# Kernel optimization log

Hardware: AMD Instinct MI355X
Metric: run time of the kernel (lower is better)

Reference implementation:

```python
import jax, jax.numpy as jnp
import numpy as np
from jax import lax

HID = 1024   # hidden_size
NH = 16      # num_heads
NKV = 4      # num_kv_heads (GQA)
HD = 64      # head_dim
SPLIT = 64   # fixed attention split size
KS = 3       # dynamic conv kernel size


def setup_inputs() -> dict:
    key = jax.random.key(0)
    ks = jax.random.split(key, 9)
    s = 0.02
    return {
        "hidden_states": jax.random.normal(ks[0], (2, 2048, HID), jnp.float32),
        "w_q": jax.random.normal(ks[1], (NH * HD, HID), jnp.float32) * s,
        "w_k": jax.random.normal(ks[2], (NKV * HD, HID), jnp.float32) * s,
        "w_v": jax.random.normal(ks[3], (NKV * HD, HID), jnp.float32) * s,
        "w_o": jax.random.normal(ks[4], (HID, NH * HD), jnp.float32) * s,
        "w_kgen": jax.random.normal(ks[5], (KS, HID), jnp.float32) * s,   # kernel_gen Linear weight
        "b_kgen": jnp.zeros((KS,), jnp.float32),
        "w_conv": jax.random.normal(ks[6], (HID, 1, KS), jnp.float32) * s,  # depthwise conv (O, I/g=1, K)
        "b_conv": jnp.zeros((HID,), jnp.float32),
    }


def _dynamic_conv(x, w_kgen, b_kgen, w_conv, b_conv):
    # x: (B, S, H). context-adaptive scalar gate per batch item (strict path:
    # per-item sigmoid(dyn_weights).mean() is a scalar -> vectorized identically).
    context = x.mean(axis=1)                                   # (B, H)
    dyn = context @ w_kgen.T + b_kgen                          # (B, KS)
    gate = jax.nn.sigmoid(dyn).mean(axis=1)                    # (B,)
    x_t = x.transpose(0, 2, 1)                                 # (B, H, S)
    y = lax.conv_general_dilated(
        x_t, w_conv, window_strides=(1,), padding=[(KS // 2, KS // 2)],
        feature_group_count=HID, dimension_numbers=("NCH", "OIH", "NCH"))
    y = (y + b_conv[None, :, None]) * gate[:, None, None]      # (B, H, S)
    return y.transpose(0, 2, 1)                                # (B, S, H)


def _fixed_split_attention(x, w_q, w_k, w_v, w_o):
    B, S, _ = x.shape
    q = (x @ w_q.T).reshape(B, S, NH, HD).transpose(0, 2, 1, 3)    # (B, NH, S, D)
    k = (x @ w_k.T).reshape(B, S, NKV, HD).transpose(0, 2, 1, 3)   # (B, NKV, S, D)
    v = (x @ w_v.T).reshape(B, S, NKV, HD).transpose(0, 2, 1, 3)
    n_rep = NH // NKV
    k = jnp.repeat(k, n_rep, axis=1)                               # GQA repeat
    v = jnp.repeat(v, n_rep, axis=1)
    C = S // SPLIT                                                 # number of KV chunks
    kc = k.reshape(B, NH, C, SPLIT, HD)
    vc = v.reshape(B, NH, C, SPLIT, HD)
    scale = HD ** -0.5
    # chunk-local softmax (NOT a global softmax) -- faithful to strict path
    scores = jnp.einsum("bhqd,bhckd->bhcqk", q, kc) * scale        # (B,NH,C,S,SPLIT)
    w = jax.nn.softmax(scores.astype(jnp.float32), axis=-1).astype(q.dtype)
    chunk_out = jnp.einsum("bhcqk,bhckd->bhcqd", w, vc)            # (B,NH,C,S,D)
    sum_w = w.sum(axis=-1, keepdims=True)                          # (B,NH,C,S,1) ~= 1
    combined = (chunk_out * sum_w).sum(axis=2)                     # (B,NH,S,D)
    total = sum_w.sum(axis=2)                                      # (B,NH,S,1)
    out = combined / (total + 1e-9)
    out = out.transpose(0, 2, 1, 3).reshape(B, S, NH * HD)
    return out @ w_o.T


def reference(hidden_states, w_q, w_k, w_v, w_o, w_kgen, b_kgen, w_conv, b_conv):
    h = _dynamic_conv(hidden_states, w_kgen, b_kgen, w_conv, b_conv)
    return _fixed_split_attention(h, w_q, w_k, w_v, w_o)
```

## Files before the change

### kernel.cpp

```cpp
#include <hip/hip_runtime.h>
#include <hip/hip_bf16.h>

#define S_LEN 2048
#define HIDN 1024
#define NCHUNK 32
#define QKN 1280

typedef __attribute__((ext_vector_type(8))) short bf16x8;
typedef __attribute__((ext_vector_type(4))) float f32x4;

__device__ __forceinline__ unsigned short f2bf(float f) {
  unsigned u = __float_as_uint(f);
  u += 0x7FFF + ((u >> 16) & 1);
  return (unsigned short)(u >> 16);
}

__device__ __forceinline__ int swz(int row, int col) {
  int u = ((col >> 3) ^ row ^ (row >> 3)) & 7;
  return row * 64 + (u << 3) + (col & 7);
}

__device__ __forceinline__ void gload_lds16(const void* g, void* l) {
  __builtin_amdgcn_global_load_lds(
      (const __attribute__((address_space(1))) unsigned int*)g,
      (__attribute__((address_space(3))) unsigned int*)l, 16, 0, 0);
}

__global__ __launch_bounds__(256) void ctx_partial_kernel(const float* __restrict__ x,
                                                          float* __restrict__ ctx) {
  int b = blockIdx.y, sc = blockIdx.x, t = threadIdx.x;
  float a0 = 0, a1 = 0, a2 = 0, a3 = 0;
  const float* base = x + ((size_t)b * S_LEN + sc * 32) * HIDN;
  for (int s = 0; s < 32; ++s) {
    const float* r = base + (size_t)s * HIDN;
    a0 += r[t]; a1 += r[t + 256]; a2 += r[t + 512]; a3 += r[t + 768];
  }
  atomicAdd(&ctx[b * HIDN + t], a0);
  atomicAdd(&ctx[b * HIDN + t + 256], a1);
  atomicAdd(&ctx[b * HIDN + t + 512], a2);
  atomicAdd(&ctx[b * HIDN + t + 768], a3);
}

__global__ __launch_bounds__(256) void gate_kernel(const float* __restrict__ ctx,
                                                   const float* __restrict__ w_kgen,
                                                   const float* __restrict__ b_kgen,
                                                   float* __restrict__ gate) {
  int b = blockIdx.x, t = threadIdx.x;
  __shared__ float red[256];
  float p[3] = {0.f, 0.f, 0.f};
  for (int c = t; c < 1024; c += 256) {
    float cv = ctx[b * HIDN + c] * (1.0f / 2048.0f);
    p[0] += cv * w_kgen[c];
    p[1] += cv * w_kgen[1024 + c];
    p[2] += cv * w_kgen[2048 + c];
  }
  float g = 0.f;
  for (int j = 0; j < 3; ++j) {
    red[t] = p[j];
    __syncthreads();
    for (int s = 128; s > 0; s >>= 1) {
      if (t < s) red[t] += red[t + s];
      __syncthreads();
    }
    if (t == 0) g += 1.0f / (1.0f + expf(-(red[0] + b_kgen[j])));
    __syncthreads();
  }
  if (t == 0) gate[b] = g * (1.0f / 3.0f);
}

__global__ __launch_bounds__(256) void conv_kernel(const float* __restrict__ x,
                                                   const float* __restrict__ w_conv,
                                                   const float* __restrict__ b_conv,
                                                   const float* __restrict__ gate,
                                                   unsigned short* __restrict__ hbuf) {
  int e = (blockIdx.x * 256 + threadIdx.x) * 4;
  int row = e >> 10, h0 = e & 1023;
  int s = row & (S_LEN - 1), b = row >> 11;
  const float* xr = x + (size_t)row * HIDN + h0;
  float xc[4], xm[4] = {0, 0, 0, 0}, xp[4] = {0, 0, 0, 0};
  *(float4*)xc = *(const float4*)xr;
  if (s > 0) *(float4*)xm = *(const float4*)(xr - HIDN);
  if (s < S_LEN - 1) *(float4*)xp = *(const float4*)(xr + HIDN);
  float g = gate[b];
  ushort4 o;
  unsigned short ov[4];
#pragma unroll
  for (int j = 0; j < 4; ++j) {
    int hh = h0 + j;
    float v = xm[j] * w_conv[hh * 3] + xc[j] * w_conv[hh * 3 + 1] +
              xp[j] * w_conv[hh * 3 + 2] + b_conv[hh];
    ov[j] = f2bf(v * g);
  }
  o.x = ov[0]; o.y = ov[1]; o.z = ov[2]; o.w = ov[3];
  *(ushort4*)(hbuf + e) = o;
}

__global__ __launch_bounds__(256) void wcast_kernel(const float* __restrict__ wq,
                                                    const float* __restrict__ wk,
                                                    const float* __restrict__ wv,
                                                    const float* __restrict__ wo,
                                                    unsigned short* __restrict__ W) {
  int e = (blockIdx.x * 256 + threadIdx.x) * 4;
  int row = e >> 10, col = e & 1023;
  const float* src;
  if (row < 1024) src = wq + (size_t)row * 1024 + col;
  else if (row < 1280) src = wk + (size_t)(row - 1024) * 1024 + col;
  else if (row < 1536) src = wv + (size_t)(row - 1280) * 1024 + col;
  else src = wo + (size_t)(row - 1536) * 1024 + col;
  float v[4];
  *(float4*)v = *(const float4*)src;
  ushort4 o;
  o.x = f2bf(v[0]); o.y = f2bf(v[1]); o.z = f2bf(v[2]); o.w = f2bf(v[3]);
  *(ushort4*)(W + e) = o;
}

template <int MODE>
__global__ __launch_bounds__(256) void gemm_bt(const unsigned short* __restrict__ A,
                                               const unsigned short* __restrict__ Bw,
                                               void* __restrict__ Cv,
                                               unsigned short* __restrict__ vt,
                                               int ldc) {
  __shared__ __align__(16) unsigned short As[128 * 32];
  __shared__ __align__(16) unsigned short Bs[128 * 32];
  const int t = threadIdx.x, w = t >> 6, l = t & 63;
  const int wr = w >> 1, wc = w & 1;
  const int tM = blockIdx.y * 128, tN = blockIdx.x * 128;
  const int lr = l >> 2, lc = (l & 3) * 8;
  f32x4 acc[4][4] = {};
  for (int k0 = 0; k0 < 1024; k0 += 32) {
#pragma unroll
    for (int i = 0; i < 2; ++i) {
      int seg = i * 4 + w;
      gload_lds16(A + (size_t)(tM + seg * 16 + lr) * 1024 + k0 + lc, &As[seg * 512]);
      gload_lds16(Bw + (size_t)(tN + seg * 16 + lr) * 1024 + k0 + lc, &Bs[seg * 512]);
    }
    __syncthreads();
    bf16x8 a[4], b[4];
#pragma unroll
    for (int m = 0; m < 4; ++m)
      a[m] = *(const bf16x8*)&As[(wr * 64 + m * 16 + (l & 15)) * 32 + (l >> 4) * 8];
#pragma unroll
    for (int n = 0; n < 4; ++n)
      b[n] = *(const bf16x8*)&Bs[(wc * 64 + n * 16 + (l & 15)) * 32 + (l >> 4) * 8];
#pragma unroll
    for (int m = 0; m < 4; ++m)
#pragma unroll
      for (int n = 0; n < 4; ++n)
        acc[m][n] = __builtin_amdgcn_mfma_f32_16x16x32_bf16(a[m], b[n], acc[m][n], 0, 0, 0);
    __syncthreads();
  }
  if constexpr (MODE == 1) {
    if (tN >= 1280) {
#pragma unroll
      for (int m = 0; m < 4; ++m)
#pragma unroll
        for (int n = 0; n < 4; ++n) {
          int d = (tN - 1280) + wc * 64 + n * 16 + (l & 15);
          int kvh = d >> 6, dl = d & 63;
          int srow = tM + wr * 64 + m * 16 + (l >> 4) * 4;
          int bb = srow >> 11, s = srow & (S_LEN - 1);
          ushort4 o;
          o.x = f2bf(acc[m][n][0]); o.y = f2bf(acc[m][n][1]);
          o.z = f2bf(acc[m][n][2]); o.w = f2bf(acc[m][n][3]);
          *(ushort4*)&vt[((size_t)((bb * 4 + kvh) * 64 + dl) << 11) + s] = o;
        }
    } else {
      unsigned short* C = (unsigned short*)Cv;
      const float sc = (tN < 1024) ? 0.18033688011112042f : 1.0f;
#pragma unroll
      for (int m = 0; m < 4; ++m)
#pragma unroll
        for (int n = 0; n < 4; ++n)
#pragma unroll
          for (int r = 0; r < 4; ++r) {
            int row = tM + wr * 64 + m * 16 + (l >> 4) * 4 + r;
            int col = tN + wc * 64 + n * 16 + (l & 15);
            C[(size_t)row * ldc + col] = f2bf(acc[m][n][r] * sc);
          }
    }
  } else {
    float* C = (float*)Cv;
#pragma unroll
    for (int m = 0; m < 4; ++m)
#pragma unroll
      for (int n = 0; n < 4; ++n)
#pragma unroll
        for (int r = 0; r < 4; ++r) {
          int row = tM + wr * 64 + m * 16 + (l >> 4) * 4 + r;
          int col = tN + wc * 64 + n * 16 + (l & 15);
          C[(size_t)row * ldc + col] = acc[m][n][r];
        }
  }
}

#define STAGE(cc, bb)                                                      \
  do {                                                                     \
    gload_lds16(kg0 + (size_t)(cc) * (64 * QKN), &ks[bb][w * 512]);        \
    gload_lds16(kg1 + (size_t)(cc) * (64 * QKN), &ks[bb][2048 + w * 512]); \
    gload_lds16(vg0 + (cc) * 64, &vs[bb][w * 512]);                        \
    gload_lds16(vg1 + (cc) * 64, &vs[bb][2048 + w * 512]);                 \
  } while (0)

__global__ __launch_bounds__(256, 4) void attn_kernel(const unsigned short* __restrict__ qkv,
                                                      const unsigned short* __restrict__ vt,
                                                      unsigned short* __restrict__ attn) {
  const int qt = blockIdx.x, head = blockIdx.y, b = blockIdx.z;
  const int t = threadIdx.x, w = t >> 6, l = t & 63;
  const int hi = l >> 4, lo = l & 15;
  const int kv = head >> 2;
  __shared__ __align__(16) unsigned short ks[2][4096];
  __shared__ __align__(16) unsigned short vs[2][4096];
  __shared__ __align__(16) unsigned int psd[2048];

  const unsigned short* qp =
      qkv + (size_t)(b * S_LEN + qt * 64 + w * 16 + lo) * QKN + head * 64;
  bf16x8 qa[2];
  qa[0] = *(const bf16x8*)(qp + hi * 8);
  qa[1] = *(const bf16x8*)(qp + 32 + hi * 8);

  const int r0 = t >> 3, u0 = t & 7, r1 = r0 + 32;
  const int x0 = (r0 ^ (r0 >> 3)) & 7, x1 = (r1 ^ (r1 >> 3)) & 7;
  const unsigned short* kg0 =
      qkv + (size_t)(b * S_LEN + r0) * QKN + 1024 + kv * 64 + ((u0 ^ x0) << 3);
  const unsigned short* kg1 =
      qkv + (size_t)(b * S_LEN + r1) * QKN + 1024 + kv * 64 + ((u0 ^ x1) << 3);
  const unsigned short* vg0 =
      vt + (size_t)((b * 4 + kv) * 64 + r0) * S_LEN + ((u0 ^ x0) << 3);
  const unsigned short* vg1 =
      vt + (size_t)((b * 4 + kv) * 64 + r1) * S_LEN + ((u0 ^ x1) << 3);

  int pre[4][2];
#pragma unroll
  for (int f = 0; f < 4; ++f) {
    int row = f * 16 + lo, rx = (row ^ (row >> 3)) & 7;
#pragma unroll
    for (int kk = 0; kk < 2; ++kk) pre[f][kk] = row * 64 + (((kk * 4 + hi) ^ rx) << 3);
  }
  const int key = (lo >> 1) << 2;
  const int Xw = w * 512 + ((lo * 32 + hi * 2) ^ key);
  const int Rb0 = w * 512 + lo * 32 + ((hi * 4) ^ key);
  const int Rb1 = w * 512 + lo * 32 + ((16 + hi * 4) ^ key);

  STAGE(0, 0);
  __syncthreads();

  f32x4 oacc[4] = {};
  int buf = 0;
  for (int c = 0; c < NCHUNK; ++c) {
    if (c + 1 < NCHUNK) STAGE(c + 1, buf ^ 1);
    const unsigned short* kb = ks[buf];
    const unsigned short* vb = vs[buf];
    f32x4 sacc[4] = {};
#pragma unroll
    for (int kk = 0; kk < 2; ++kk)
#pragma unroll
      for (int f = 0; f < 4; ++f)
        sacc[f] = __builtin_amdgcn_mfma_f32_16x16x32_bf16(
            *(const bf16x8*)&kb[pre[f][kk]], qa[kk], sacc[f], 0, 0, 0);
    float pv[4][4], ssum = 0.f;
#pragma unroll
    for (int f = 0; f < 4; ++f)
#pragma unroll
      for (int r = 0; r < 4; ++r) {
        pv[f][r] = __builtin_amdgcn_exp2f(sacc[f][r]);
        ssum += pv[f][r];
      }
    ssum += __shfl_xor(ssum, 16);
    ssum += __shfl_xor(ssum, 32);
    const float inv = __builtin_amdgcn_rcpf(ssum);
#pragma unroll
    for (int f = 0; f < 4; ++f)
#pragma unroll
      for (int rr = 0; rr < 2; ++rr) {
        __hip_bfloat162 h2 = __float22bfloat162_rn(
            make_float2(pv[f][2 * rr] * inv, pv[f][2 * rr + 1] * inv));
        psd[Xw ^ (f * 8 + rr)] = *(unsigned*)&h2;
      }
    bf16x8 pa0 = *(const bf16x8*)&psd[Rb0];
    bf16x8 pa1 = *(const bf16x8*)&psd[Rb1];
#pragma unroll
    for (int f = 0; f < 4; ++f) {
      oacc[f] = __builtin_amdgcn_mfma_f32_16x16x32_bf16(
          pa0, *(const bf16x8*)&vb[pre[f][0]], oacc[f], 0, 0, 0);
      oacc[f] = __builtin_amdgcn_mfma_f32_16x16x32_bf16(
          pa1, *(const bf16x8*)&vb[pre[f][1]], oacc[f], 0, 0, 0);
    }
    __syncthreads();
    buf ^= 1;
  }

  const float invC = 1.0f / 32.0f;
#pragma unroll
  for (int f = 0; f < 4; ++f)
#pragma unroll
    for (int r = 0; r < 4; ++r) {
      int row = b * S_LEN + qt * 64 + w * 16 + hi * 4 + r;
      int col = head * 64 + f * 16 + lo;
      attn[(size_t)row * HIDN + col] = f2bf(oacc[f][r] * invC);
    }
}
#undef STAGE

extern "C" void kernel_launch(void* const* d_in, const int* in_sizes, int n_in,
                              void* d_out, int out_size, void* d_ws, size_t ws_size,
                              hipStream_t stream) {
  const float* x = (const float*)d_in[0];
  const float* w_q = (const float*)d_in[1];
  const float* w_k = (const float*)d_in[2];
  const float* w_v = (const float*)d_in[3];
  const float* w_o = (const float*)d_in[4];
  const float* w_kgen = (const float*)d_in[5];
  const float* b_kgen = (const float*)d_in[6];
  const float* w_conv = (const float*)d_in[7];
  const float* b_conv = (const float*)d_in[8];
  float* out = (float*)d_out;

  char* ws = (char*)d_ws;
  float* ctx = (float*)ws;
  float* gate = (float*)(ws + 8192);
  unsigned short* W = (unsigned short*)(ws + 65536);
  unsigned short* h = (unsigned short*)(ws + 6291456);
  unsigned short* qkv = (unsigned short*)(ws + 14680064);
  unsigned short* vt = (unsigned short*)(ws + 25165824);
  unsigned short* attnb = h;

  hipMemsetAsync(ctx, 0, 8192, stream);
  ctx_partial_kernel<<<dim3(64, 2), 256, 0, stream>>>(x, ctx);
  gate_kernel<<<2, 256, 0, stream>>>(ctx, w_kgen, b_kgen, gate);
  conv_kernel<<<4096, 256, 0, stream>>>(x, w_conv, b_conv, gate, h);
  wcast_kernel<<<2560, 256, 0, stream>>>(w_q, w_k, w_v, w_o, W);
  gemm_bt<1><<<dim3(12, 32), 256, 0, stream>>>(h, W, qkv, vt, QKN);
  attn_kernel<<<dim3(32, 16, 2), 256, 0, stream>>>(qkv, vt, attnb);
  gemm_bt<0><<<dim3(8, 32), 256, 0, stream>>>(attnb, W + 1536 * 1024, out, nullptr, HIDN);
}
```

Measured before the change: 218.2 us.

## Split KV chunks across waves with direct global fragment loads and LDS reduction

The attention kernel stops having each wave own 16 query rows and walk all 32 KV chunks through double-buffered shared memory. Now each wave owns all 64 query rows and processes every fourth chunk, loading K and V fragments straight from global memory into registers. The four waves' partial outputs are summed through a shared-memory reduction at the end. This removes the per-chunk block barriers and staging traffic, and reuses K/V fragments across four query groups. In exchange it uses far more registers (occupancy hint lowered to 2) and loses the async LDS prefetch overlap.

```diff
diff --git a/kernel.cpp b/kernel.cpp
--- a/kernel.cpp
+++ b/kernel.cpp
@@ -13,11 +13,6 @@
   unsigned u = __float_as_uint(f);
   u += 0x7FFF + ((u >> 16) & 1);
   return (unsigned short)(u >> 16);
-}
-
-__device__ __forceinline__ int swz(int row, int col) {
-  int u = ((col >> 3) ^ row ^ (row >> 3)) & 7;
-  return row * 64 + (u << 3) + (col & 7);
 }
 
 __device__ __forceinline__ void gload_lds16(const void* g, void* l) {
@@ -193,113 +188,135 @@
   }
 }
 
-#define STAGE(cc, bb)                                                      \
-  do {                                                                     \
-    gload_lds16(kg0 + (size_t)(cc) * (64 * QKN), &ks[bb][w * 512]);        \
-    gload_lds16(kg1 + (size_t)(cc) * (64 * QKN), &ks[bb][2048 + w * 512]); \
-    gload_lds16(vg0 + (cc) * 64, &vs[bb][w * 512]);                        \
-    gload_lds16(vg1 + (cc) * 64, &vs[bb][2048 + w * 512]);                 \
-  } while (0)
-
-__global__ __launch_bounds__(256, 4) void attn_kernel(const unsigned short* __restrict__ qkv,
+__global__ __launch_bounds__(256, 2) void attn_kernel(const unsigned short* __restrict__ qkv,
                                                       const unsigned short* __restrict__ vt,
                                                       unsigned short* __restrict__ attn) {
   const int qt = blockIdx.x, head = blockIdx.y, b = blockIdx.z;
   const int t = threadIdx.x, w = t >> 6, l = t & 63;
   const int hi = l >> 4, lo = l & 15;
   const int kv = head >> 2;
-  __shared__ __align__(16) unsigned short ks[2][4096];
-  __shared__ __align__(16) unsigned short vs[2][4096];
-  __shared__ __align__(16) unsigned int psd[2048];
-
-  const unsigned short* qp =
-      qkv + (size_t)(b * S_LEN + qt * 64 + w * 16 + lo) * QKN + head * 64;
-  bf16x8 qa[2];
-  qa[0] = *(const bf16x8*)(qp + hi * 8);
-  qa[1] = *(const bf16x8*)(qp + 32 + hi * 8);
-
-  const int r0 = t >> 3, u0 = t & 7, r1 = r0 + 32;
-  const int x0 = (r0 ^ (r0 >> 3)) & 7, x1 = (r1 ^ (r1 >> 3)) & 7;
-  const unsigned short* kg0 =
-      qkv + (size_t)(b * S_LEN + r0) * QKN + 1024 + kv * 64 + ((u0 ^ x0) << 3);
-  const unsigned short* kg1 =
-      qkv + (size_t)(b * S_LEN + r1) * QKN + 1024 + kv * 64 + ((u0 ^ x1) << 3);
-  const unsigned short* vg0 =
-      vt + (size_t)((b * 4 + kv) * 64 + r0) * S_LEN + ((u0 ^ x0) << 3);
-  const unsigned short* vg1 =
-      vt + (size_t)((b * 4 + kv) * 64 + r1) * S_LEN + ((u0 ^ x1) << 3);
-
-  int pre[4][2];
-#pragma unroll
-  for (int f = 0; f < 4; ++f) {
-    int row = f * 16 + lo, rx = (row ^ (row >> 3)) & 7;
-#pragma unroll
-    for (int kk = 0; kk < 2; ++kk) pre[f][kk] = row * 64 + (((kk * 4 + hi) ^ rx) << 3);
-  }
-  const int key = (lo >> 1) << 2;
-  const int Xw = w * 512 + ((lo * 32 + hi * 2) ^ key);
-  const int Rb0 = w * 512 + lo * 32 + ((hi * 4) ^ key);
-  const int Rb1 = w * 512 + lo * 32 + ((16 + hi * 4) ^ key);
-
-  STAGE(0, 0);
+  __shared__ __align__(16) float red[4][4096];
+  unsigned* psd = (unsigned*)&red[w][0];
+
+  bf16x8 qb[4][2];
+  const unsigned short* qbase =
+      qkv + (size_t)(b * S_LEN + qt * 64 + lo) * QKN + head * 64 + hi * 8;
+#pragma unroll
+  for (int qg = 0; qg < 4; ++qg)
+#pragma unroll
+    for (int kk = 0; kk < 2; ++kk)
+      qb[qg][kk] = *(const bf16x8*)(qbase + qg * 16 * QKN + kk * 32);
+
+  const unsigned short* kbase = qkv + (size_t)(b * S_LEN + lo) * QKN + 1024 + kv * 64 + hi * 8;
+  const unsigned short* vbase = vt + (size_t)((b * 4 + kv) * 64 + lo) * S_LEN + hi * 8;
+  const int key = (lo & 7) << 2;
+
+  f32x4 oacc[4][4] = {};
+
+  for (int c = w; c < NCHUNK; c += 4) {
+    const unsigned short* kc = kbase + (size_t)c * (64 * QKN);
+    bf16x8 kf[4][2];
+#pragma unroll
+    for (int f = 0; f < 4; ++f)
+#pragma unroll
+      for (int kk = 0; kk < 2; ++kk)
+        kf[f][kk] = *(const bf16x8*)(kc + f * (16 * QKN) + kk * 32);
+
+    f32x4 sacc[4][4] = {};
+#pragma unroll
+    for (int kk = 0; kk < 2; ++kk)
+#pragma unroll
+      for (int f = 0; f < 4; ++f)
+#pragma unroll
+        for (int qg = 0; qg < 4; ++qg)
+          sacc[f][qg] = __builtin_amdgcn_mfma_f32_16x16x32_bf16(kf[f][kk], qb[qg][kk],
+                                                               sacc[f][qg], 0, 0, 0);
+
+    const unsigned short* vc = vbase + c * 64;
+    bf16x8 vf[4][2];
+#pragma unroll
+    for (int fd = 0; fd < 4; ++fd)
+#pragma unroll
+      for (int kk = 0; kk < 2; ++kk)
+        vf[fd][kk] = *(const bf16x8*)(vc + fd * (16 * S_LEN) + kk * 32);
+
+    float ssum[4] = {0.f, 0.f, 0.f, 0.f};
+#pragma unroll
+    for (int f = 0; f < 4; ++f)
+#pragma unroll
+      for (int qg = 0; qg < 4; ++qg)
+#pragma unroll
+        for (int r = 0; r < 4; ++r) {
+          sacc[f][qg][r] = __builtin_amdgcn_exp2f(sacc[f][qg][r]);
+          ssum[qg] += sacc[f][qg][r];
+        }
+#pragma unroll
+    for (int qg = 0; qg < 4; ++qg) {
+      ssum[qg] += __shfl_xor(ssum[qg], 16);
+      ssum[qg] += __shfl_xor(ssum[qg], 32);
+      ssum[qg] = __builtin_amdgcn_rcpf(ssum[qg]);
+    }
+
+#pragma unroll
+    for (int qg = 0; qg < 4; ++qg) {
+      const int qrow = (qg * 16 + lo) * 32;
+#pragma unroll
+      for (int f = 0; f < 4; ++f) {
+        __hip_bfloat162 p01 = __float22bfloat162_rn(
+            make_float2(sacc[f][qg][0] * ssum[qg], sacc[f][qg][1] * ssum[qg]));
+        __hip_bfloat162 p23 = __float22bfloat162_rn(
+            make_float2(sacc[f][qg][2] * ssum[qg], sacc[f][qg][3] * ssum[qg]));
+        uint2 d;
+        d.x = *(unsigned*)&p01; d.y = *(unsigned*)&p23;
+        *(uint2*)&psd[qrow + ((f * 8 + hi * 2) ^ key)] = d;
+      }
+    }
+
+#pragma unroll
+    for (int qg = 0; qg < 4; ++qg) {
+      const int qrow = (qg * 16 + lo) * 32;
+      bf16x8 pa0 = *(const bf16x8*)&psd[qrow + ((hi * 4) ^ key)];
+      bf16x8 pa1 = *(const bf16x8*)&psd[qrow + ((16 + hi * 4) ^ key)];
+#pragma unroll
+      for (int fd = 0; fd < 4; ++fd) {
+        oacc[qg][fd] = __builtin_amdgcn_mfma_f32_16x16x32_bf16(pa0, vf[fd][0],
+                                                              oacc[qg][fd], 0, 0, 0);
+        oacc[qg][fd] = __builtin_amdgcn_mfma_f32_16x16x32_bf16(pa1, vf[fd][1],
+                                                              oacc[qg][fd], 0, 0, 0);
+      }
+    }
+  }
+
+#pragma unroll
+  for (int qg = 0; qg < 4; ++qg)
+#pragma unroll
+    for (int f = 0; f < 4; ++f)
+#pragma unroll
+      for (int r = 0; r < 4; ++r)
+        red[w][(qg * 16 + hi * 4 + r) * 64 + f * 16 + lo] = oacc[qg][f][r];
   __syncthreads();
-
-  f32x4 oacc[4] = {};
-  int buf = 0;
-  for (int c = 0; c < NCHUNK; ++c) {
-    if (c + 1 < NCHUNK) STAGE(c + 1, buf ^ 1);
-    const unsigned short* kb = ks[buf];
-    const unsigned short* vb = vs[buf];
-    f32x4 sacc[4] = {};
-#pragma unroll
-    for (int kk = 0; kk < 2; ++kk)
-#pragma unroll
-      for (int f = 0; f < 4; ++f)
-        sacc[f] = __builtin_amdgcn_mfma_f32_16x16x32_bf16(
-            *(const bf16x8*)&kb[pre[f][kk]], qa[kk], sacc[f], 0, 0, 0);
-    float pv[4][4], ssum = 0.f;
-#pragma unroll
-    for (int f = 0; f < 4; ++f)
-#pragma unroll
-      for (int r = 0; r < 4; ++r) {
-        pv[f][r] = __builtin_amdgcn_exp2f(sacc[f][r]);
-        ssum += pv[f][r];
+  {
+    const int q = t >> 2, d0 = (t & 3) * 16;
+    float acc16[16];
+#pragma unroll
+    for (int j = 0; j < 16; ++j) acc16[j] = 0.f;
+#pragma unroll
+    for (int ww = 0; ww < 4; ++ww)
+#pragma unroll
+      for (int j4 = 0; j4 < 4; ++j4) {
+        f32x4 v4 = *(const f32x4*)&red[ww][q * 64 + d0 + j4 * 4];
+#pragma unroll
+        for (int i = 0; i < 4; ++i) acc16[j4 * 4 + i] += v4[i];
       }
-    ssum += __shfl_xor(ssum, 16);
-    ssum += __shfl_xor(ssum, 32);
-    const float inv = __builtin_amdgcn_rcpf(ssum);
-#pragma unroll
-    for (int f = 0; f < 4; ++f)
-#pragma unroll
-      for (int rr = 0; rr < 2; ++rr) {
-        __hip_bfloat162 h2 = __float22bfloat162_rn(
-            make_float2(pv[f][2 * rr] * inv, pv[f][2 * rr + 1] * inv));
-        psd[Xw ^ (f * 8 + rr)] = *(unsigned*)&h2;
-      }
-    bf16x8 pa0 = *(const bf16x8*)&psd[Rb0];
-    bf16x8 pa1 = *(const bf16x8*)&psd[Rb1];
-#pragma unroll
-    for (int f = 0; f < 4; ++f) {
-      oacc[f] = __builtin_amdgcn_mfma_f32_16x16x32_bf16(
-          pa0, *(const bf16x8*)&vb[pre[f][0]], oacc[f], 0, 0, 0);
-      oacc[f] = __builtin_amdgcn_mfma_f32_16x16x32_bf16(
-          pa1, *(const bf16x8*)&vb[pre[f][1]], oacc[f], 0, 0, 0);
-    }
-    __syncthreads();
-    buf ^= 1;
-  }
-
-  const float invC = 1.0f / 32.0f;
-#pragma unroll
-  for (int f = 0; f < 4; ++f)
-#pragma unroll
-    for (int r = 0; r < 4; ++r) {
-      int row = b * S_LEN + qt * 64 + w * 16 + hi * 4 + r;
-      int col = head * 64 + f * 16 + lo;
-      attn[(size_t)row * HIDN + col] = f2bf(oacc[f][r] * invC);
-    }
-}
-#undef STAGE
+    unsigned short o16[16];
+#pragma unroll
+    for (int j = 0; j < 16; ++j) o16[j] = f2bf(acc16[j] * (1.0f / 32.0f));
+    size_t row = (size_t)(b * S_LEN + qt * 64 + q);
+    unsigned short* dst = attn + row * HIDN + head * 64 + d0;
+    *(uint4*)dst = ((const uint4*)o16)[0];
+    *(uint4*)(dst + 8) = ((const uint4*)o16)[1];
+  }
+}
 
 extern "C" void kernel_launch(void* const* d_in, const int* in_sizes, int n_in,
                               void* d_out, int out_size, void* d_ws, size_t ws_size,
```

New measurement: 222.0 us. Within noise of the previous version (+1.8%).
